# Performance work log

Measured on AMD Instinct MI355X. Metric: run time of the kernel, lower is better.

Reference implementation:

```python
import jax, jax.numpy as jnp
import numpy as np

SCALE = 4          # sigma // 2 with sigma = 8
EP = 1e-20         # epsilon used by xcorr_torch


def _pad(x, w):
    # zero-pad last two (spatial) dims by w on each side
    cfg = [(0, 0)] * (x.ndim - 2) + [(w, w), (w, w)]
    return jnp.pad(x, cfg)


def _box(x, w):
    # sliding 2w x 2w box sum via 2D integral image (cumsum trick),
    # matching xcorr_torch's cumsum/difference formulation.
    c = jnp.cumsum(jnp.cumsum(x, axis=-1), axis=-2)
    return (c[..., 2 * w:, 2 * w:] - c[..., :-2 * w, 2 * w:]
            - c[..., 2 * w:, :-2 * w] + c[..., :-2 * w, :-2 * w])


def _xcorr(a, b, w):
    # local (windowed) normalized cross-correlation field.
    # a: [B,C,1,H,W], b: [B,1,L,H,W]; broadcasting gives [B,C,L,H,W]
    a_mu = _box(_pad(a, w), w) / (4.0 * w * w)
    b_mu = _box(_pad(b, w), w) / (4.0 * w * w)
    ac = _pad(a - a_mu, w)
    bc = _pad(b - b_mu, w)
    sii = jnp.maximum(_box(ac * ac, w), EP)   # clip lower bound; upper clip at
    sjj = jnp.maximum(_box(bc * bc, w), EP)   # tensor max in torch is a no-op
    sij = _box(ac * bc, w)                    # [B,C,L,H,W]
    return sij / (jnp.sqrt(sii * sjj) + EP)


def setup_inputs() -> dict:
    key = jax.random.key(0)
    k1, k2 = jax.random.split(key)
    outputs = jax.random.uniform(k1, (4, 6, 512, 512), dtype=jnp.float32)
    labels = jax.random.uniform(k2, (4, 4, 512, 512), dtype=jnp.float32)
    return {"outputs": outputs, "labels": labels}


def reference(outputs, labels):
    w = SCALE
    a = outputs[:, :, None]            # [B,C,1,H,W]
    b = labels[:, None, :]             # [B,1,L,H,W]
    cc = _xcorr(a, b, w)               # [B,C,L,H,W] (torch loop over L, vectorized)
    Y = jnp.maximum(cc, -1.0)          # torch.clamp(min=-1)
    Y = jnp.max(Y, axis=2)             # amax over label channels -> [B,C,H,W]
    Y = jnp.clip(Y, -1.0, 1.0)
    X = 1.0 - Y
    return (jnp.mean(X), jnp.mean(X, axis=(2, 3)))
```

## Files before the change

### kernel.cpp

```cpp
#include <hip/hip_runtime.h>
#include <hip/hip_fp16.h>

#define HH 512
#define WW 512
#define HW (HH*WW)
#define EPV 1e-20f


__device__ __forceinline__ float bpl(int addr, float v) {
    return __int_as_float(__builtin_amdgcn_ds_bpermute(addr, __float_as_int(v)));
}
__device__ __forceinline__ int rcl(int r) { return min(max(r, 0), HH - 1); }

__device__ __forceinline__ float4 h2f4(uint2 r) {
    __half2 lo = *(__half2*)&r.x, hi = *(__half2*)&r.y;
    float2 a = __half22float2(lo), b = __half22float2(hi);
    return make_float4(a.x, a.y, b.x, b.y);
}
__device__ __forceinline__ uint2 f2h4(float4 v) {
    __half2 lo = __floats2half2_rn(v.x, v.y);
    __half2 hi = __floats2half2_rn(v.z, v.w);
    uint2 r;
    r.x = *(unsigned int*)&lo;
    r.y = *(unsigned int*)&hi;
    return r;
}
__device__ __forceinline__ uint4 pack8(float4 a, float4 b) {
    uint2 lo = f2h4(a), hi = f2h4(b);
    return make_uint4(lo.x, lo.y, hi.x, hi.y);
}
__device__ __forceinline__ void unpack8(uint4 r, float4& a, float4& b) {
    a = h2f4(make_uint2(r.x, r.y));
    b = h2f4(make_uint2(r.z, r.w));
}

__global__ void __launch_bounds__(64)
__attribute__((amdgpu_waves_per_eu(3, 3)))
prep_f8(const float* __restrict__ outs, const float* __restrict__ labs,
        __half* __restrict__ ac, __half* __restrict__ rs,
        float* __restrict__ wsum)
{
    const int l = threadIdx.x;
    if (blockIdx.x == 0 && blockIdx.y == 0 && l < 24)
        wsum[l * 64] = 0.f;
    const int y0 = 8 * blockIdx.x;
    const int z  = blockIdx.y;

    const float* src = (z < 24) ? outs + z * HW : labs + (z - 24) * HW;
    __half* acd = ac + z * HW;
    __half* rsd = rs + z * HW;

    const int   col = 8 * l;
    const int   aL1 = ((l - 1) & 63) << 2;
    const int   aR1 = ((l + 1) & 63) << 2;
    const float lmE = (l > 0)  ? 1.f : 0.f;
    const float rmE = (l < 63) ? 1.f : 0.f;

    float4 rgA[8], rgB[8];
    float4 fOA[2], fOB[2];
    uint4  pk[8];
    float4 VAa = {0,0,0,0}, VAb = {0,0,0,0};
    float4 Vqa = {0,0,0,0}, Vqb = {0,0,0,0};
    #pragma unroll
    for (int k = 0; k < 8; ++k) {
        rgA[k] = make_float4(0,0,0,0); rgB[k] = make_float4(0,0,0,0);
        pk[k]  = make_uint4(0,0,0,0);
    }
    fOA[0] = fOA[1] = fOB[0] = fOB[1] = make_float4(0,0,0,0);
    rgA[0] = *(const float4*)&src[rcl(y0 - 7) * WW + col];
    rgB[0] = *(const float4*)&src[rcl(y0 - 7) * WW + col + 4];
    rgA[1] = *(const float4*)&src[rcl(y0 - 6) * WW + col];
    rgB[1] = *(const float4*)&src[rcl(y0 - 6) * WW + col + 4];

    auto step = [&](const int t) {
        const int   r  = y0 - 7 + t;
        const float rm = (r >= 0 && r < HH) ? 1.f : 0.f;
        {
            float4 ra = rgA[t & 7], rb = rgB[t & 7];
            VAa.x += ra.x*rm; VAa.y += ra.y*rm; VAa.z += ra.z*rm; VAa.w += ra.w*rm;
            VAb.x += rb.x*rm; VAb.y += rb.y*rm; VAb.z += rb.z*rm; VAb.w += rb.w*rm;
        }
        if (t >= 8) {
            const float rm8 = ((r - 8) >= 0 && (r - 8) < HH) ? 1.f : 0.f;
            float4 oa = fOA[t & 1], ob = fOB[t & 1];
            VAa.x -= oa.x*rm8; VAa.y -= oa.y*rm8; VAa.z -= oa.z*rm8; VAa.w -= oa.w*rm8;
            VAb.x -= ob.x*rm8; VAb.y -= ob.y*rm8; VAb.z -= ob.z*rm8; VAb.w -= ob.w*rm8;
        }
        if (t <= 20) {
            const int rn = rcl(r + 2);
            rgA[(t + 2) & 7] = *(const float4*)&src[rn * WW + col];
            rgB[(t + 2) & 7] = *(const float4*)&src[rn * WW + col + 4];
        }
        if (t >= 6 && t <= 20) {
            const int ro = rcl(r - 6);
            fOA[t & 1] = *(const float4*)&src[ro * WW + col];
            fOB[t & 1] = *(const float4*)&src[ro * WW + col + 4];
        }
        if (t >= 8) {
            const int   c  = r - 4;
            const float cm = (c >= 0 && c < HH) ? 1.f : 0.f;
            float p1 = VAa.x, p2 = p1+VAa.y, p3 = p2+VAa.z, p4 = p3+VAa.w;
            float p5 = p4+VAb.x, p6 = p5+VAb.y, p7 = p6+VAb.z, tt = p7+VAb.w;
            float s1 = VAb.w, s2 = VAb.z+s1, s3 = VAb.y+s2;
            float L1 = bpl(aL1, s1)*lmE, L2 = bpl(aL1, s2)*lmE, L3 = bpl(aL1, s3)*lmE;
            float R1 = bpl(aR1, p1)*rmE, R2 = bpl(aR1, p2)*rmE;
            float R3 = bpl(aR1, p3)*rmE, R4 = bpl(aR1, p4)*rmE;
            float4 rc0 = rgA[(t + 4) & 7], rc1 = rgB[(t + 4) & 7];
            float4 aL4, aH4;
            aL4.x = (rc0.x - (L3+p5)    * (1.f/64.f)) * cm;
            aL4.y = (rc0.y - (L2+p6)    * (1.f/64.f)) * cm;
            aL4.z = (rc0.z - (L1+p7)    * (1.f/64.f)) * cm;
            aL4.w = (rc0.w - tt         * (1.f/64.f)) * cm;
            aH4.x = (rc1.x - (tt-p1+R1) * (1.f/64.f)) * cm;
            aH4.y = (rc1.y - (tt-p2+R2) * (1.f/64.f)) * cm;
            aH4.z = (rc1.z - (tt-p3+R3) * (1.f/64.f)) * cm;
            aH4.w = (rc1.w - (tt-p4+R4) * (1.f/64.f)) * cm;
            uint4 pkNew = pack8(aL4, aH4);
            if (t >= 11 && t <= 18)
                *(uint4*)&acd[c * WW + col] = pkNew;
            float4 qnL, qnH; unpack8(pkNew, qnL, qnH);
            Vqa.x += qnL.x*qnL.x; Vqa.y += qnL.y*qnL.y;
            Vqa.z += qnL.z*qnL.z; Vqa.w += qnL.w*qnL.w;
            Vqb.x += qnH.x*qnH.x; Vqb.y += qnH.y*qnH.y;
            Vqb.z += qnH.z*qnH.z; Vqb.w += qnH.w*qnH.w;
            if (t >= 16) {
                float4 oL, oH; unpack8(pk[t & 7], oL, oH);
                Vqa.x -= oL.x*oL.x; Vqa.y -= oL.y*oL.y;
                Vqa.z -= oL.z*oL.z; Vqa.w -= oL.w*oL.w;
                Vqb.x -= oH.x*oH.x; Vqb.y -= oH.y*oH.y;
                Vqb.z -= oH.z*oH.z; Vqb.w -= oH.w*oH.w;
            }
            pk[t & 7] = pkNew;
            if (t >= 15 && t <= 22) {
                const int y = c - 4;
                float q1 = Vqa.x, q2 = q1+Vqa.y, q3 = q2+Vqa.z, q4 = q3+Vqa.w;
                float q5 = q4+Vqb.x, q6 = q5+Vqb.y, q7 = q6+Vqb.z, qt = q7+Vqb.w;
                float z1 = Vqb.w, z2 = Vqb.z+z1, z3 = Vqb.y+z2;
                float Lq1 = bpl(aL1, z1)*lmE, Lq2 = bpl(aL1, z2)*lmE, Lq3 = bpl(aL1, z3)*lmE;
                float Rq1 = bpl(aR1, q1)*rmE, Rq2 = bpl(aR1, q2)*rmE;
                float Rq3 = bpl(aR1, q3)*rmE, Rq4 = bpl(aR1, q4)*rmE;
                float4 rL, rH;
                rL.x = fminf(__frsqrt_rn(fmaxf(Lq3+q5,    EPV)), 60000.f);
                rL.y = fminf(__frsqrt_rn(fmaxf(Lq2+q6,    EPV)), 60000.f);
                rL.z = fminf(__frsqrt_rn(fmaxf(Lq1+q7,    EPV)), 60000.f);
                rL.w = fminf(__frsqrt_rn(fmaxf(qt,        EPV)), 60000.f);
                rH.x = fminf(__frsqrt_rn(fmaxf(qt-q1+Rq1, EPV)), 60000.f);
                rH.y = fminf(__frsqrt_rn(fmaxf(qt-q2+Rq2, EPV)), 60000.f);
                rH.z = fminf(__frsqrt_rn(fmaxf(qt-q3+Rq3, EPV)), 60000.f);
                rH.w = fminf(__frsqrt_rn(fmaxf(qt-q4+Rq4, EPV)), 60000.f);
                *(uint4*)&rsd[y * WW + col] = pack8(rL, rH);
            }
        }
    };
    #pragma unroll
    for (int t = 0; t < 23; ++t) step(t);
}

__global__ void __launch_bounds__(64)
__attribute__((amdgpu_waves_per_eu(2, 2)))
ncc_f8(const __half* __restrict__ ac, const __half* __restrict__ rs,
       float* __restrict__ wsum)
{
    const int l   = threadIdx.x;
    const int n   = blockIdx.x;
    const int xcd = n & 7;
    const int p   = n >> 3;
    const int zq  = p >> 6;
    const int seg = p & 63;
    const int z   = 3 * xcd + zq;
    const int b   = z / 6;
    const int y0  = 8 * seg;

    const __half* acp = ac + z * HW;
    const __half* sip = rs + z * HW;
    const __half* bcp[4]; const __half* sjp[4];
    #pragma unroll
    for (int j = 0; j < 4; ++j) {
        bcp[j] = ac + (24 + b * 4 + j) * HW;
        sjp[j] = rs + (24 + b * 4 + j) * HW;
    }

    const int   col = 8 * l;
    const int   aL1 = ((l - 1) & 63) << 2;
    const int   aR1 = ((l + 1) & 63) << 2;
    const float lmE = (l > 0)  ? 1.f : 0.f;
    const float rmE = (l < 63) ? 1.f : 0.f;

    uint4 fa[2], fb[4][2];
    uint4 oA[2], oB[4][2];
    {
        const int r0 = rcl(y0 - 3), r1 = rcl(y0 - 2);
        fa[0] = *(const uint4*)&acp[r0 * WW + col];
        fa[1] = *(const uint4*)&acp[r1 * WW + col];
        #pragma unroll
        for (int j = 0; j < 4; ++j) {
            fb[j][0] = *(const uint4*)&bcp[j][r0 * WW + col];
            fb[j][1] = *(const uint4*)&bcp[j][r1 * WW + col];
            oB[j][0] = make_uint4(0,0,0,0); oB[j][1] = make_uint4(0,0,0,0);
        }
        oA[0] = make_uint4(0,0,0,0); oA[1] = make_uint4(0,0,0,0);
    }

    float4 VpL[4], VpH[4];
    uint4 psiB[2], psjB[2][4];
    float4 xsL = make_float4(0,0,0,0), xsH = make_float4(0,0,0,0);
    #pragma unroll
    for (int j = 0; j < 4; ++j) {
        VpL[j] = make_float4(0,0,0,0); VpH[j] = make_float4(0,0,0,0);
        psjB[0][j] = make_uint4(0,0,0,0); psjB[1][j] = make_uint4(0,0,0,0);
    }
    psiB[0] = make_uint4(0,0,0,0); psiB[1] = make_uint4(0,0,0,0);

    auto step = [&](const int t) {
        const int   c  = y0 - 3 + t;
        const float rm = (c >= 0 && c < HH) ? 1.f : 0.f;
        uint4 ar = fa[t & 1];
        uint4 br0 = fb[0][t & 1], br1 = fb[1][t & 1];
        uint4 br2 = fb[2][t & 1], br3 = fb[3][t & 1];
        uint4 arO = oA[t & 1];
        uint4 bo0 = oB[0][t & 1], bo1 = oB[1][t & 1];
        uint4 bo2 = oB[2][t & 1], bo3 = oB[3][t & 1];
        if (t <= 12) {
            const int rn = rcl(c + 2);
            fa[t & 1] = *(const uint4*)&acp[rn * WW + col];
            #pragma unroll
            for (int j = 0; j < 4; ++j)
                fb[j][t & 1] = *(const uint4*)&bcp[j][rn * WW + col];
        }
        if (t >= 6 && t <= 12) {
            const int ro = rcl(c - 6);
            oA[t & 1] = *(const uint4*)&acp[ro * WW + col];
            #pragma unroll
            for (int j = 0; j < 4; ++j)
                oB[j][t & 1] = *(const uint4*)&bcp[j][ro * WW + col];
        }
        {
            float4 avL, avH; unpack8(ar, avL, avH);
            avL.x *= rm; avL.y *= rm; avL.z *= rm; avL.w *= rm;
            avH.x *= rm; avH.y *= rm; avH.z *= rm; avH.w *= rm;
            float4 bL, bH;
            unpack8(br0, bL, bH);
            VpL[0].x += avL.x*bL.x; VpL[0].y += avL.y*bL.y; VpL[0].z += avL.z*bL.z; VpL[0].w += avL.w*bL.w;
            VpH[0].x += avH.x*bH.x; VpH[0].y += avH.y*bH.y; VpH[0].z += avH.z*bH.z; VpH[0].w += avH.w*bH.w;
            unpack8(br1, bL, bH);
            VpL[1].x += avL.x*bL.x; VpL[1].y += avL.y*bL.y; VpL[1].z += avL.z*bL.z; VpL[1].w += avL.w*bL.w;
            VpH[1].x += avH.x*bH.x; VpH[1].y += avH.y*bH.y; VpH[1].z += avH.z*bH.z; VpH[1].w += avH.w*bH.w;
            unpack8(br2, bL, bH);
            VpL[2].x += avL.x*bL.x; VpL[2].y += avL.y*bL.y; VpL[2].z += avL.z*bL.z; VpL[2].w += avL.w*bL.w;
            VpH[2].x += avH.x*bH.x; VpH[2].y += avH.y*bH.y; VpH[2].z += avH.z*bH.z; VpH[2].w += avH.w*bH.w;
            unpack8(br3, bL, bH);
            VpL[3].x += avL.x*bL.x; VpL[3].y += avL.y*bL.y; VpL[3].z += avL.z*bL.z; VpL[3].w += avL.w*bL.w;
            VpH[3].x += avH.x*bH.x; VpH[3].y += avH.y*bH.y; VpH[3].z += avH.z*bH.z; VpH[3].w += avH.w*bH.w;
        }
        if (t >= 8) {
            const float rmO = ((c - 8) >= 0) ? 1.f : 0.f;
            float4 avL, avH; unpack8(arO, avL, avH);
            avL.x *= rmO; avL.y *= rmO; avL.z *= rmO; avL.w *= rmO;
            avH.x *= rmO; avH.y *= rmO; avH.z *= rmO; avH.w *= rmO;
            float4 bL, bH;
            unpack8(bo0, bL, bH);
            VpL[0].x -= avL.x*bL.x; VpL[0].y -= avL.y*bL.y; VpL[0].z -= avL.z*bL.z; VpL[0].w -= avL.w*bL.w;
            VpH[0].x -= avH.x*bH.x; VpH[0].y -= avH.y*bH.y; VpH[0].z -= avH.z*bH.z; VpH[0].w -= avH.w*bH.w;
            unpack8(bo1, bL, bH);
            VpL[1].x -= avL.x*bL.x; VpL[1].y -= avL.y*bL.y; VpL[1].z -= avL.z*bL.z; VpL[1].w -= avL.w*bL.w;
            VpH[1].x -= avH.x*bH.x; VpH[1].y -= avH.y*bH.y; VpH[1].z -= avH.z*bH.z; VpH[1].w -= avH.w*bH.w;
            unpack8(bo2, bL, bH);
            VpL[2].x -= avL.x*bL.x; VpL[2].y -= avL.y*bL.y; VpL[2].z -= avL.z*bL.z; VpL[2].w -= avL.w*bL.w;
            VpH[2].x -= avH.x*bH.x; VpH[2].y -= avH.y*bH.y; VpH[2].z -= avH.z*bH.z; VpH[2].w -= avH.w*bH.w;
            unpack8(bo3, bL, bH);
            VpL[3].x -= avL.x*bL.x; VpL[3].y -= avL.y*bL.y; VpL[3].z -= avL.z*bL.z; VpL[3].w -= avL.w*bL.w;
            VpH[3].x -= avH.x*bH.x; VpH[3].y -= avH.y*bH.y; VpH[3].z -= avH.z*bH.z; VpH[3].w -= avH.w*bH.w;
        }
        if (t >= 7 && t <= 14) {
            float4 pL, pH; unpack8(psiB[t & 1], pL, pH);
            float4 mmL = make_float4(-1,-1,-1,-1), mmH = make_float4(-1,-1,-1,-1);
            #pragma unroll
            for (int j = 0; j < 4; ++j) {
                float q1 = VpL[j].x, q2 = q1+VpL[j].y, q3 = q2+VpL[j].z, q4 = q3+VpL[j].w;
                float q5 = q4+VpH[j].x, q6 = q5+VpH[j].y, q7 = q6+VpH[j].z, q8 = q7+VpH[j].w;
                float s1 = VpH[j].w, s2 = VpH[j].z+s1, s3 = VpH[j].y+s2;
                float L1 = bpl(aL1, s1)*lmE, L2 = bpl(aL1, s2)*lmE, L3 = bpl(aL1, s3)*lmE;
                float R1 = bpl(aR1, q1)*rmE, R2 = bpl(aR1, q2)*rmE;
                float R3 = bpl(aR1, q3)*rmE, R4 = bpl(aR1, q4)*rmE;
                float4 sL, sH; unpack8(psjB[t & 1][j], sL, sH);
                mmL.x = fmaxf(mmL.x, (L3+q5)    * (pL.x*sL.x));
                mmL.y = fmaxf(mmL.y, (L2+q6)    * (pL.y*sL.y));
                mmL.z = fmaxf(mmL.z, (L1+q7)    * (pL.z*sL.z));
                mmL.w = fmaxf(mmL.w, q8         * (pL.w*sL.w));
                mmH.x = fmaxf(mmH.x, (q8-q1+R1) * (pH.x*sH.x));
                mmH.y = fmaxf(mmH.y, (q8-q2+R2) * (pH.y*sH.y));
                mmH.z = fmaxf(mmH.z, (q8-q3+R3) * (pH.z*sH.z));
                mmH.w = fmaxf(mmH.w, (q8-q4+R4) * (pH.w*sH.w));
            }
            xsL.x += 1.f - fminf(mmL.x, 1.f);
            xsL.y += 1.f - fminf(mmL.y, 1.f);
            xsL.z += 1.f - fminf(mmL.z, 1.f);
            xsL.w += 1.f - fminf(mmL.w, 1.f);
            xsH.x += 1.f - fminf(mmH.x, 1.f);
            xsH.y += 1.f - fminf(mmH.y, 1.f);
            xsH.z += 1.f - fminf(mmH.z, 1.f);
            xsH.w += 1.f - fminf(mmH.w, 1.f);
        }
        if (t >= 5 && t <= 12) {
            const int yn = min(y0 + t - 5, HH - 1);
            psiB[t & 1] = *(const uint4*)&sip[yn * WW + col];
            #pragma unroll
            for (int j = 0; j < 4; ++j)
                psjB[t & 1][j] = *(const uint4*)&sjp[j][yn * WW + col];
        }
    };
    #pragma unroll
    for (int t = 0; t < 15; ++t) step(t);

    float xt = xsL.x + xsL.y + xsL.z + xsL.w + xsH.x + xsH.y + xsH.z + xsH.w;
    #pragma unroll
    for (int off = 32; off > 0; off >>= 1) xt += __shfl_down(xt, off);
    if (l == 0) atomicAdd(&wsum[z * 64], xt);
}

__global__ void fin_f4(const float* __restrict__ wsum, float* __restrict__ out)
{
    const int l = threadIdx.x;
    float v = (l < 24) ? wsum[l * 64] : 0.f;
    if (l < 24) out[1 + l] = v * (1.f / (float)HW);
    #pragma unroll
    for (int off = 32; off > 0; off >>= 1) v += __shfl_down(v, off);
    if (l == 0) out[0] = v * (1.f / (24.f * (float)HW));
}

extern "C" void kernel_launch(void* const* d_in, const int* in_sizes, int n_in,
                              void* d_out, int out_size, void* d_ws, size_t ws_size,
                              hipStream_t stream) {
    const float* outs = (const float*)d_in[0];
    const float* labs = (const float*)d_in[1];
    float* out = (float*)d_out;
    float* ws  = (float*)d_ws;

    __half* acw  = (__half*)ws;
    __half* rsw  = (__half*)ws + 40 * HW;
    float*  wsum = ws + 40 * HW;

    prep_f8<<<dim3(64, 40), 64, 0, stream>>>(outs, labs, acw, rsw, wsum);
    ncc_f8<<<dim3(1536, 1, 1), 64, 0, stream>>>(acw, rsw, wsum);
    fin_f4<<<dim3(1, 1, 1), 64, 0, stream>>>(wsum, out);
}
```

Before: 129.8 us.

## Double prep rows per block and keep a packed fp16 row ring

After: 112.5 us. -13.3%, faster.

```diff
diff --git a/kernel.cpp b/kernel.cpp
--- a/kernel.cpp
+++ b/kernel.cpp
@@ -35,7 +35,7 @@
 }
 
 __global__ void __launch_bounds__(64)
-__attribute__((amdgpu_waves_per_eu(3, 3)))
+__attribute__((amdgpu_waves_per_eu(2, 2)))
 prep_f8(const float* __restrict__ outs, const float* __restrict__ labs,
         __half* __restrict__ ac, __half* __restrict__ rs,
         float* __restrict__ wsum)
@@ -43,7 +43,7 @@
     const int l = threadIdx.x;
     if (blockIdx.x == 0 && blockIdx.y == 0 && l < 24)
         wsum[l * 64] = 0.f;
-    const int y0 = 8 * blockIdx.x;
+    const int y0 = 16 * blockIdx.x;
     const int z  = blockIdx.y;
 
     const float* src = (z < 24) ? outs + z * HW : labs + (z - 24) * HW;
@@ -56,45 +56,40 @@
     const float lmE = (l > 0)  ? 1.f : 0.f;
     const float rmE = (l < 63) ? 1.f : 0.f;
 
-    float4 rgA[8], rgB[8];
-    float4 fOA[2], fOB[2];
-    uint4  pk[8];
+    auto ldpack = [&](int row) {
+        float4 a = *(const float4*)&src[row * WW + col];
+        float4 b = *(const float4*)&src[row * WW + col + 4];
+        return pack8(a, b);
+    };
+
+    uint4 rg[13];
+    uint4 pk[8];
     float4 VAa = {0,0,0,0}, VAb = {0,0,0,0};
     float4 Vqa = {0,0,0,0}, Vqb = {0,0,0,0};
     #pragma unroll
-    for (int k = 0; k < 8; ++k) {
-        rgA[k] = make_float4(0,0,0,0); rgB[k] = make_float4(0,0,0,0);
-        pk[k]  = make_uint4(0,0,0,0);
-    }
-    fOA[0] = fOA[1] = fOB[0] = fOB[1] = make_float4(0,0,0,0);
-    rgA[0] = *(const float4*)&src[rcl(y0 - 7) * WW + col];
-    rgB[0] = *(const float4*)&src[rcl(y0 - 7) * WW + col + 4];
-    rgA[1] = *(const float4*)&src[rcl(y0 - 6) * WW + col];
-    rgB[1] = *(const float4*)&src[rcl(y0 - 6) * WW + col + 4];
+    for (int k = 0; k < 13; ++k) rg[k] = make_uint4(0,0,0,0);
+    #pragma unroll
+    for (int k = 0; k < 8; ++k) pk[k] = make_uint4(0,0,0,0);
+    rg[0] = ldpack(rcl(y0 - 7));
+    rg[1] = ldpack(rcl(y0 - 6));
+    rg[2] = ldpack(rcl(y0 - 5));
 
     auto step = [&](const int t) {
         const int   r  = y0 - 7 + t;
         const float rm = (r >= 0 && r < HH) ? 1.f : 0.f;
         {
-            float4 ra = rgA[t & 7], rb = rgB[t & 7];
+            float4 ra, rb; unpack8(rg[t % 13], ra, rb);
             VAa.x += ra.x*rm; VAa.y += ra.y*rm; VAa.z += ra.z*rm; VAa.w += ra.w*rm;
             VAb.x += rb.x*rm; VAb.y += rb.y*rm; VAb.z += rb.z*rm; VAb.w += rb.w*rm;
         }
         if (t >= 8) {
             const float rm8 = ((r - 8) >= 0 && (r - 8) < HH) ? 1.f : 0.f;
-            float4 oa = fOA[t & 1], ob = fOB[t & 1];
+            float4 oa, ob; unpack8(rg[(t - 8) % 13], oa, ob);
             VAa.x -= oa.x*rm8; VAa.y -= oa.y*rm8; VAa.z -= oa.z*rm8; VAa.w -= oa.w*rm8;
             VAb.x -= ob.x*rm8; VAb.y -= ob.y*rm8; VAb.z -= ob.z*rm8; VAb.w -= ob.w*rm8;
         }
-        if (t <= 20) {
-            const int rn = rcl(r + 2);
-            rgA[(t + 2) & 7] = *(const float4*)&src[rn * WW + col];
-            rgB[(t + 2) & 7] = *(const float4*)&src[rn * WW + col + 4];
-        }
-        if (t >= 6 && t <= 20) {
-            const int ro = rcl(r - 6);
-            fOA[t & 1] = *(const float4*)&src[ro * WW + col];
-            fOB[t & 1] = *(const float4*)&src[ro * WW + col + 4];
+        if (t <= 27) {
+            rg[(t + 3) % 13] = ldpack(rcl(y0 - 4 + t));
         }
         if (t >= 8) {
             const int   c  = r - 4;
@@ -105,7 +100,7 @@
             float L1 = bpl(aL1, s1)*lmE, L2 = bpl(aL1, s2)*lmE, L3 = bpl(aL1, s3)*lmE;
             float R1 = bpl(aR1, p1)*rmE, R2 = bpl(aR1, p2)*rmE;
             float R3 = bpl(aR1, p3)*rmE, R4 = bpl(aR1, p4)*rmE;
-            float4 rc0 = rgA[(t + 4) & 7], rc1 = rgB[(t + 4) & 7];
+            float4 rc0, rc1; unpack8(rg[(t - 4) % 13], rc0, rc1);
             float4 aL4, aH4;
             aL4.x = (rc0.x - (L3+p5)    * (1.f/64.f)) * cm;
             aL4.y = (rc0.y - (L2+p6)    * (1.f/64.f)) * cm;
@@ -116,7 +111,7 @@
             aH4.z = (rc1.z - (tt-p3+R3) * (1.f/64.f)) * cm;
             aH4.w = (rc1.w - (tt-p4+R4) * (1.f/64.f)) * cm;
             uint4 pkNew = pack8(aL4, aH4);
-            if (t >= 11 && t <= 18)
+            if (t >= 11 && t <= 26)
                 *(uint4*)&acd[c * WW + col] = pkNew;
             float4 qnL, qnH; unpack8(pkNew, qnL, qnH);
             Vqa.x += qnL.x*qnL.x; Vqa.y += qnL.y*qnL.y;
@@ -131,7 +126,7 @@
                 Vqb.z -= oH.z*oH.z; Vqb.w -= oH.w*oH.w;
             }
             pk[t & 7] = pkNew;
-            if (t >= 15 && t <= 22) {
+            if (t >= 15 && t <= 30) {
                 const int y = c - 4;
                 float q1 = Vqa.x, q2 = q1+Vqa.y, q3 = q2+Vqa.z, q4 = q3+Vqa.w;
                 float q5 = q4+Vqb.x, q6 = q5+Vqb.y, q7 = q6+Vqb.z, qt = q7+Vqb.w;
@@ -153,7 +148,7 @@
         }
     };
     #pragma unroll
-    for (int t = 0; t < 23; ++t) step(t);
+    for (int t = 0; t < 31; ++t) step(t);
 }
 
 __global__ void __launch_bounds__(64)
@@ -340,7 +335,7 @@
     __half* rsw  = (__half*)ws + 40 * HW;
     float*  wsum = ws + 40 * HW;
 
-    prep_f8<<<dim3(64, 40), 64, 0, stream>>>(outs, labs, acw, rsw, wsum);
+    prep_f8<<<dim3(32, 40), 64, 0, stream>>>(outs, labs, acw, rsw, wsum);
     ncc_f8<<<dim3(1536, 1, 1), 64, 0, stream>>>(acw, rsw, wsum);
     fin_f4<<<dim3(1, 1, 1), 64, 0, stream>>>(wsum, out);
 }
```
